# Optimization experiments

Measured on AMD Instinct MI355X. Metric: run time of the kernel, lower is better.

The kernel has to match this reference:

```python
import jax, jax.numpy as jnp
import numpy as np

EMBED_DIM = 1024
B, QL, KL = 4, 2048, 2048

def setup_inputs() -> dict:
    key = jax.random.key(0)
    k1, k2, k3, k4 = jax.random.split(key, 4)
    hidden_states = jax.random.normal(k1, (B, QL, EMBED_DIM), dtype=jnp.float32)
    decoder_hidden_states = jax.random.normal(k2, (B, KL, EMBED_DIM), dtype=jnp.float32)
    # Linear weights stored as [in, out] (torch stores [out, in]; math identical via x @ W)
    Wq = jax.random.normal(k3, (EMBED_DIM, EMBED_DIM), dtype=jnp.float32) * (1.0 / np.sqrt(EMBED_DIM))
    Wkv = jax.random.normal(k4, (EMBED_DIM, 2 * EMBED_DIM), dtype=jnp.float32) * (1.0 / np.sqrt(EMBED_DIM))
    return {"hidden_states": hidden_states, "decoder_hidden_states": decoder_hidden_states,
            "Wq": Wq, "Wkv": Wkv}

def reference(hidden_states, decoder_hidden_states, Wq, Wkv):
    d = Wq.shape[0]
    scale = 1.0 / np.sqrt(d)
    query = hidden_states @ Wq                      # [B, QL, D]
    kv = decoder_hidden_states @ Wkv                # [B, KL, 2D]
    key, value = jnp.split(kv, 2, axis=-1)          # each [B, KL, D]
    scores = jnp.einsum('bqd,bkd->bqk', query, key) * scale  # [B, QL, KL]
    w = jax.nn.softmax(scores, axis=-1)
    return jnp.einsum('bqk,bkd->bqd', w, value)     # [B, QL, D]
```

## Files before the change

kernel.cpp:

```cpp
#include <hip/hip_runtime.h>
#include <stdint.h>


typedef __bf16 bf16_t;
typedef __bf16 bf16x8 __attribute__((ext_vector_type(8)));
typedef __bf16 bf16x4 __attribute__((ext_vector_type(4)));
typedef float  f32x4  __attribute__((ext_vector_type(4)));

#define MFMA_BF16(A, B, C) __builtin_amdgcn_mfma_f32_16x16x32_bf16((A), (B), (C), 0, 0, 0)
#define ATTN_SHIFT 16.0f

__device__ __forceinline__ void async_copy16(const void* g, void* l) {
  __builtin_amdgcn_global_load_lds(
      (const __attribute__((address_space(1))) uint32_t*)g,
      (__attribute__((address_space(3))) uint32_t*)l, 16, 0, 0);
}

#define PH_PRE()                                             \
  do {                                                       \
    __builtin_amdgcn_sched_barrier(0);                       \
    __builtin_amdgcn_s_barrier();                            \
    asm volatile("s_waitcnt lgkmcnt(0)" ::: "memory");       \
    __builtin_amdgcn_sched_barrier(0);                       \
    __builtin_amdgcn_s_setprio(1);                           \
  } while (0)
#define PH_POST()                                            \
  do {                                                       \
    __builtin_amdgcn_s_setprio(0);                           \
    __builtin_amdgcn_sched_barrier(0);                       \
    __builtin_amdgcn_s_barrier();                            \
  } while (0)

__global__ void zero_f32_kernel(float* __restrict__ p, int n) {
  int i = blockIdx.x * blockDim.x + threadIdx.x;
  if (i < n) p[i] = 0.f;
}

__global__ void cast_bf16_kernel(const float* __restrict__ in, bf16_t* __restrict__ out, int n) {
  int idx = (blockIdx.x * blockDim.x + threadIdx.x) * 4;
  int stride = gridDim.x * blockDim.x * 4;
  for (int i = idx; i < n; i += stride) {
    float4 v = *(const float4*)(in + i);
    bf16x4 o;
    o[0] = (bf16_t)v.x; o[1] = (bf16_t)v.y; o[2] = (bf16_t)v.z; o[3] = (bf16_t)v.w;
    *(bf16x4*)(out + i) = o;
  }
}

__global__ void transpose_cast_kernel(const float* __restrict__ src, bf16_t* __restrict__ dst,
                                      int R, int C, float scale) {
  __shared__ float tile[32][33];
  int c0 = blockIdx.x * 32, r0 = blockIdx.y * 32;
  int tx = threadIdx.x, ty = threadIdx.y;
#pragma unroll
  for (int i = 0; i < 4; ++i) {
    int r = ty + i * 8;
    tile[r][tx] = src[(size_t)(r0 + r) * C + c0 + tx] * scale;
  }
  __syncthreads();
#pragma unroll
  for (int i = 0; i < 4; ++i) {
    int c = ty + i * 8;
    dst[(size_t)(c0 + c) * R + r0 + tx] = (bf16_t)tile[tx][c];
  }
}

template <int BN, int EPI>
__global__ __launch_bounds__(512, 2) void gemm8(
    const bf16_t* __restrict__ A, int lda, size_t sA,
    const bf16_t* __restrict__ Bt, int ldb, size_t sB,
    void* __restrict__ Cv, int ldc, size_t sC,
    void* __restrict__ Cv2, int nb, int K, float* __restrict__ rowsum) {
  constexpr int ABYTES = 256 * 64 * 2;
  constexpr int BBYTES = BN * 64 * 2;
  constexpr int NCF = BN / 64;
  __shared__ char smem[2 * ABYTES + 2 * BBYTES];

  const int bx = blockIdx.x, bz = blockIdx.z;
  const bf16_t* Ab = A + (size_t)bz * sA;
  const bf16_t* Bb = Bt + (size_t)bz * sB;
  const int m0 = (bx / nb) << 8;
  const int n0 = (bx % nb) * BN;
  const int tid = threadIdx.x, w = tid >> 6, l = tid & 63;
  const int l15 = l & 15, l4 = l >> 4;
  const int wr = w >> 2, wc = w & 3;
  const int NT = K >> 6;

  const int lrow = l >> 3;
  const int gcol = ((l & 7) ^ lrow) << 3;
  const bf16_t* PA = Ab + (size_t)(m0 + 8 * w + lrow) * lda + gcol;
  const bf16_t* PB = Bb + (size_t)(n0 + 8 * w + lrow) * ldb + gcol;

  const int sw16 = (l15 & 7) << 4;
  const int aoff0 = (wr * 128 + l15) * 128;
  const int boff0 = (wc * (BN / 4) + l15) * 128;

  f32x4 acc[8][NCF] = {};
  bf16x8 af[4][2], bfr[NCF][2];

  auto stageA = [&](int t, int h) {
    if (t >= NT) return;
    const bf16_t* s = PA + (size_t)(h * 128) * lda + (t << 6);
    char* d = smem + (t & 1) * ABYTES + h * 16384 + w * 1024;
    async_copy16(s, d);
    async_copy16(s + (size_t)64 * lda, d + 8192);
  };
  auto stageB = [&](int t, int h) {
    if (t >= NT) return;
    const bf16_t* s = PB + (size_t)(h * (BN / 2)) * ldb + (t << 6);
    char* d = smem + 2 * ABYTES + (t & 1) * BBYTES + h * (BBYTES / 2) + w * 1024;
    async_copy16(s, d);
    if constexpr (BN == 256) async_copy16(s + (size_t)64 * ldb, d + 8192);
  };

  stageB(0, 0); stageA(0, 0); stageA(0, 1); stageB(0, 1);
  __builtin_amdgcn_sched_barrier(0);
  stageB(1, 0); stageA(1, 0);
  __builtin_amdgcn_sched_barrier(0);
  if constexpr (BN == 256) asm volatile("s_waitcnt vmcnt(4)" ::: "memory");
  else                     asm volatile("s_waitcnt vmcnt(3)" ::: "memory");
  __builtin_amdgcn_s_barrier();

  for (int t = 0; t < NT; ++t) {
    const int cur = t & 1;
    const char* Ac = smem + cur * ABYTES;
    const char* Bc = smem + 2 * ABYTES + cur * BBYTES;
#pragma unroll
    for (int rf = 0; rf < 4; ++rf)
#pragma unroll
      for (int kh = 0; kh < 2; ++kh)
        af[rf][kh] = *(const bf16x8*)(Ac + aoff0 + rf * 2048 + ((((kh * 4 + l4) << 4)) ^ sw16));
#pragma unroll
    for (int cf = 0; cf < NCF / 2; ++cf)
#pragma unroll
      for (int kh = 0; kh < 2; ++kh)
        bfr[cf][kh] = *(const bf16x8*)(Bc + boff0 + cf * 2048 + ((((kh * 4 + l4) << 4)) ^ sw16));
    stageA(t + 1, 1);
    PH_PRE();
#pragma unroll
    for (int rf = 0; rf < 4; ++rf)
#pragma unroll
      for (int cf = 0; cf < NCF / 2; ++cf) {
        acc[rf][cf] = MFMA_BF16(af[rf][0], bfr[cf][0], acc[rf][cf]);
        acc[rf][cf] = MFMA_BF16(af[rf][1], bfr[cf][1], acc[rf][cf]);
      }
    PH_POST();
#pragma unroll
    for (int cf = NCF / 2; cf < NCF; ++cf)
#pragma unroll
      for (int kh = 0; kh < 2; ++kh)
        bfr[cf][kh] = *(const bf16x8*)(Bc + boff0 + cf * 2048 + ((((kh * 4 + l4) << 4)) ^ sw16));
    stageB(t + 1, 1);
    PH_PRE();
#pragma unroll
    for (int rf = 0; rf < 4; ++rf)
#pragma unroll
      for (int cf = NCF / 2; cf < NCF; ++cf) {
        acc[rf][cf] = MFMA_BF16(af[rf][0], bfr[cf][0], acc[rf][cf]);
        acc[rf][cf] = MFMA_BF16(af[rf][1], bfr[cf][1], acc[rf][cf]);
      }
    PH_POST();
#pragma unroll
    for (int rf = 0; rf < 4; ++rf)
#pragma unroll
      for (int kh = 0; kh < 2; ++kh)
        af[rf][kh] = *(const bf16x8*)(Ac + aoff0 + 8192 + rf * 2048 + ((((kh * 4 + l4) << 4)) ^ sw16));
    stageB(t + 2, 0);
    PH_PRE();
#pragma unroll
    for (int rf = 0; rf < 4; ++rf)
#pragma unroll
      for (int cf = 0; cf < NCF / 2; ++cf) {
        acc[4 + rf][cf] = MFMA_BF16(af[rf][0], bfr[cf][0], acc[4 + rf][cf]);
        acc[4 + rf][cf] = MFMA_BF16(af[rf][1], bfr[cf][1], acc[4 + rf][cf]);
      }
    PH_POST();
    stageA(t + 2, 0);
    PH_PRE();
#pragma unroll
    for (int rf = 0; rf < 4; ++rf)
#pragma unroll
      for (int cf = NCF / 2; cf < NCF; ++cf) {
        acc[4 + rf][cf] = MFMA_BF16(af[rf][0], bfr[cf][0], acc[4 + rf][cf]);
        acc[4 + rf][cf] = MFMA_BF16(af[rf][1], bfr[cf][1], acc[4 + rf][cf]);
      }
    __builtin_amdgcn_s_setprio(0);
    __builtin_amdgcn_sched_barrier(0);
    if (t < NT - 2) {
      if constexpr (BN == 256) asm volatile("s_waitcnt vmcnt(4)" ::: "memory");
      else                     asm volatile("s_waitcnt vmcnt(3)" ::: "memory");
    } else {
      asm volatile("s_waitcnt vmcnt(0)" ::: "memory");
    }
    __builtin_amdgcn_s_barrier();
  }

  __syncthreads();

  if constexpr (EPI == 0) {
    bf16_t* Cb = (bf16_t*)Cv + (size_t)bz * sC;
#pragma unroll
    for (int arf = 0; arf < 8; ++arf)
#pragma unroll
      for (int cf = 0; cf < NCF; ++cf) {
        int grow = m0 + wr * 128 + arf * 16 + l4 * 4;
        int gc = n0 + wc * (BN / 4) + cf * 16 + l15;
#pragma unroll
        for (int r = 0; r < 4; ++r)
          Cb[(size_t)(grow + r) * ldc + gc] = (bf16_t)acc[arf][cf][r];
      }
  } else if constexpr (EPI == 1) {
    bf16_t* Cb = (bf16_t*)Cv + (size_t)bz * sC;
    float* rsh = (float*)smem;
    if (tid < 256) rsh[tid] = 0.f;
    __syncthreads();
#pragma unroll
    for (int arf = 0; arf < 8; ++arf)
#pragma unroll
      for (int r = 0; r < 4; ++r) {
        int lr = wr * 128 + arf * 16 + l4 * 4 + r;
        float s = 0.f;
#pragma unroll
        for (int cf = 0; cf < NCF; ++cf) {
          float p = __expf(acc[arf][cf][r] - ATTN_SHIFT);
          bf16_t pb = (bf16_t)p;
          Cb[(size_t)(m0 + lr) * ldc + n0 + wc * (BN / 4) + cf * 16 + l15] = pb;
          s += (float)pb;
        }
        s += __shfl_xor(s, 1); s += __shfl_xor(s, 2);
        s += __shfl_xor(s, 4); s += __shfl_xor(s, 8);
        if (l15 == 0) atomicAdd(&rsh[lr], s);
      }
    __syncthreads();
    if (tid < 256) atomicAdd(&rowsum[(size_t)bz * 2048 + m0 + tid], rsh[tid]);
  } else if constexpr (EPI == 2) {
    float* rsh = (float*)smem;
    if (tid < 256) rsh[tid] = rowsum[(size_t)bz * 2048 + m0 + tid];
    __syncthreads();
    float* Cb = (float*)Cv + (size_t)bz * sC;
#pragma unroll
    for (int arf = 0; arf < 8; ++arf)
#pragma unroll
      for (int r = 0; r < 4; ++r) {
        float inv = 1.0f / rsh[wr * 128 + arf * 16 + l4 * 4 + r];
        int grow = m0 + wr * 128 + arf * 16 + l4 * 4 + r;
#pragma unroll
        for (int cf = 0; cf < NCF; ++cf)
          Cb[(size_t)grow * ldc + n0 + wc * (BN / 4) + cf * 16 + l15] = acc[arf][cf][r] * inv;
      }
  } else {
    if (n0 < 1024) {
      bf16_t* Cb = (bf16_t*)Cv;
#pragma unroll
      for (int arf = 0; arf < 8; ++arf)
#pragma unroll
        for (int cf = 0; cf < NCF; ++cf) {
          int grow = m0 + wr * 128 + arf * 16 + l4 * 4;
          int gc = n0 + wc * (BN / 4) + cf * 16 + l15;
#pragma unroll
          for (int r = 0; r < 4; ++r)
            Cb[(size_t)(grow + r) * ldc + gc] = (bf16_t)acc[arf][cf][r];
        }
    } else {
      bf16_t* VTb = (bf16_t*)Cv2;
#pragma unroll
      for (int arf = 0; arf < 8; ++arf)
#pragma unroll
        for (int cf = 0; cf < NCF; ++cf) {
          int grow0 = m0 + wr * 128 + arf * 16 + l4 * 4;
          int b = grow0 >> 11, kl = grow0 & 2047;
          int d = (n0 - 1024) + wc * (BN / 4) + cf * 16 + l15;
          bf16x4 v;
#pragma unroll
          for (int r = 0; r < 4; ++r) v[r] = (bf16_t)acc[arf][cf][r];
          *(bf16x4*)(VTb + (size_t)b * (1024 * 2048) + (size_t)d * 2048 + kl) = v;
        }
    }
  }
}

extern "C" void kernel_launch(void* const* d_in, const int* in_sizes, int n_in,
                              void* d_out, int out_size, void* d_ws, size_t ws_size,
                              hipStream_t stream) {
  const float* hs  = (const float*)d_in[0];
  const float* dhs = (const float*)d_in[1];
  const float* Wq  = (const float*)d_in[2];
  const float* Wkv = (const float*)d_in[3];
  float* out = (float*)d_out;

  const size_t M1 = 1024 * 1024;
  bf16_t* WqT  = (bf16_t*)d_ws;
  bf16_t* WkvT = WqT + M1;
  bf16_t* AB   = WkvT + 2 * M1;
  bf16_t* dhsb = AB;
  bf16_t* hsb  = AB + 8 * M1;
  bf16_t* P    = AB;
  bf16_t* Kb   = AB + 16 * M1;
  bf16_t* VTb  = Kb + 8 * M1;
  bf16_t* Qb   = VTb + 8 * M1;
  float* rowsum = (float*)(Qb + 8 * M1);

  zero_f32_kernel<<<8, 1024, 0, stream>>>(rowsum, 8192);
  cast_bf16_kernel<<<2048, 256, 0, stream>>>(dhs, dhsb, 8192 * 1024);
  cast_bf16_kernel<<<2048, 256, 0, stream>>>(hs,  hsb,  8192 * 1024);
  transpose_cast_kernel<<<dim3(32, 32), dim3(32, 8), 0, stream>>>(Wq,  WqT,  1024, 1024, 0.03125f);
  transpose_cast_kernel<<<dim3(64, 32), dim3(32, 8), 0, stream>>>(Wkv, WkvT, 1024, 2048, 1.0f);

  gemm8<256, 4><<<dim3(32 * 8, 1, 1), 512, 0, stream>>>(
      dhsb, 1024, 0, WkvT, 1024, 0, Kb, 1024, 0, VTb, 8, 1024, nullptr);
  gemm8<128, 0><<<dim3(32 * 8, 1, 1), 512, 0, stream>>>(
      hsb, 1024, 0, WqT, 1024, 0, Qb, 1024, 0, nullptr, 8, 1024, nullptr);
  gemm8<256, 1><<<dim3(64, 1, 4), 512, 0, stream>>>(
      Qb, 1024, (size_t)2048 * 1024, Kb, 1024, (size_t)2048 * 1024,
      P, 2048, (size_t)2048 * 2048, nullptr, 8, 1024, rowsum);
  gemm8<128, 2><<<dim3(64, 1, 4), 512, 0, stream>>>(
      P, 2048, (size_t)2048 * 2048, VTb, 2048, (size_t)1024 * 2048,
      out, 1024, (size_t)2048 * 1024, nullptr, 8, 2048, rowsum);
}
```

Measured before the change: 184.6 us.

## Fuse prep kernels and remap GEMM blocks across XCDs for L2 locality

Merges the rowsum zeroing and the two fp32-to-bf16 casts into one prep kernel, and the two weight transposes into one kernel, which cuts launch count. It also flattens the batch dimension into blockIdx.x and applies an XCD-aware swizzle (stride-8 interleave) so that consecutive tiles sharing A/B panels land on the same XCD's L2. The tradeoffs are extra index arithmetic and an assumption that grid size is a multiple of 8.

```diff
diff --git a/kernel.cpp b/kernel.cpp
--- a/kernel.cpp
+++ b/kernel.cpp
@@ -31,26 +31,33 @@
     __builtin_amdgcn_s_barrier();                            \
   } while (0)
 
-__global__ void zero_f32_kernel(float* __restrict__ p, int n) {
-  int i = blockIdx.x * blockDim.x + threadIdx.x;
-  if (i < n) p[i] = 0.f;
-}
-
-__global__ void cast_bf16_kernel(const float* __restrict__ in, bf16_t* __restrict__ out, int n) {
-  int idx = (blockIdx.x * blockDim.x + threadIdx.x) * 4;
+__global__ void prep_kernel(const float* __restrict__ a, const float* __restrict__ b,
+                            bf16_t* __restrict__ ab, bf16_t* __restrict__ bb,
+                            float* __restrict__ rowsum, int n) {
+  int gtid = blockIdx.x * blockDim.x + threadIdx.x;
+  if (gtid < 8192) rowsum[gtid] = 0.f;
+  int idx = gtid * 4;
   int stride = gridDim.x * blockDim.x * 4;
   for (int i = idx; i < n; i += stride) {
-    float4 v = *(const float4*)(in + i);
-    bf16x4 o;
+    float4 v = *(const float4*)(a + i);
+    float4 w = *(const float4*)(b + i);
+    bf16x4 o, p;
     o[0] = (bf16_t)v.x; o[1] = (bf16_t)v.y; o[2] = (bf16_t)v.z; o[3] = (bf16_t)v.w;
-    *(bf16x4*)(out + i) = o;
-  }
-}
-
-__global__ void transpose_cast_kernel(const float* __restrict__ src, bf16_t* __restrict__ dst,
-                                      int R, int C, float scale) {
+    p[0] = (bf16_t)w.x; p[1] = (bf16_t)w.y; p[2] = (bf16_t)w.z; p[3] = (bf16_t)w.w;
+    *(bf16x4*)(ab + i) = o;
+    *(bf16x4*)(bb + i) = p;
+  }
+}
+
+__global__ void transpose_both_kernel(const float* __restrict__ Wq, const float* __restrict__ Wkv,
+                                      bf16_t* __restrict__ WqT, bf16_t* __restrict__ WkvT) {
   __shared__ float tile[32][33];
-  int c0 = blockIdx.x * 32, r0 = blockIdx.y * 32;
+  int bx = blockIdx.x;
+  const float* src; bf16_t* dst; int R, C; float scale;
+  int cb;
+  if (bx < 32) { src = Wq;  dst = WqT;  R = 1024; C = 1024; scale = 0.03125f; cb = bx; }
+  else         { src = Wkv; dst = WkvT; R = 1024; C = 2048; scale = 1.0f;     cb = bx - 32; }
+  int c0 = cb * 32, r0 = blockIdx.y * 32;
   int tx = threadIdx.x, ty = threadIdx.y;
 #pragma unroll
   for (int i = 0; i < 4; ++i) {
@@ -70,17 +77,22 @@
     const bf16_t* __restrict__ A, int lda, size_t sA,
     const bf16_t* __restrict__ Bt, int ldb, size_t sB,
     void* __restrict__ Cv, int ldc, size_t sC,
-    void* __restrict__ Cv2, int nb, int K, float* __restrict__ rowsum) {
+    void* __restrict__ Cv2, int nb, int bpb, int K, float* __restrict__ rowsum) {
   constexpr int ABYTES = 256 * 64 * 2;
   constexpr int BBYTES = BN * 64 * 2;
   constexpr int NCF = BN / 64;
   __shared__ char smem[2 * ABYTES + 2 * BBYTES];
 
-  const int bx = blockIdx.x, bz = blockIdx.z;
+  const int bx0 = blockIdx.x;
+  const int q8 = gridDim.x >> 3;
+  const int swz = (bx0 & 7) * q8 + (bx0 >> 3);
+  const int bz = swz / bpb;
+  const int rr = swz % bpb;
+  const int m0 = (rr / nb) << 8;
+  const int n0 = (rr % nb) * BN;
+
   const bf16_t* Ab = A + (size_t)bz * sA;
   const bf16_t* Bb = Bt + (size_t)bz * sB;
-  const int m0 = (bx / nb) << 8;
-  const int n0 = (bx % nb) * BN;
   const int tid = threadIdx.x, w = tid >> 6, l = tid & 63;
   const int l15 = l & 15, l4 = l >> 4;
   const int wr = w >> 2, wc = w & 3;
@@ -300,20 +312,17 @@
   bf16_t* Qb   = VTb + 8 * M1;
   float* rowsum = (float*)(Qb + 8 * M1);
 
-  zero_f32_kernel<<<8, 1024, 0, stream>>>(rowsum, 8192);
-  cast_bf16_kernel<<<2048, 256, 0, stream>>>(dhs, dhsb, 8192 * 1024);
-  cast_bf16_kernel<<<2048, 256, 0, stream>>>(hs,  hsb,  8192 * 1024);
-  transpose_cast_kernel<<<dim3(32, 32), dim3(32, 8), 0, stream>>>(Wq,  WqT,  1024, 1024, 0.03125f);
-  transpose_cast_kernel<<<dim3(64, 32), dim3(32, 8), 0, stream>>>(Wkv, WkvT, 1024, 2048, 1.0f);
-
-  gemm8<256, 4><<<dim3(32 * 8, 1, 1), 512, 0, stream>>>(
-      dhsb, 1024, 0, WkvT, 1024, 0, Kb, 1024, 0, VTb, 8, 1024, nullptr);
-  gemm8<128, 0><<<dim3(32 * 8, 1, 1), 512, 0, stream>>>(
-      hsb, 1024, 0, WqT, 1024, 0, Qb, 1024, 0, nullptr, 8, 1024, nullptr);
-  gemm8<256, 1><<<dim3(64, 1, 4), 512, 0, stream>>>(
+  prep_kernel<<<2048, 256, 0, stream>>>(dhs, hs, dhsb, hsb, rowsum, 8192 * 1024);
+  transpose_both_kernel<<<dim3(96, 32), dim3(32, 8), 0, stream>>>(Wq, Wkv, WqT, WkvT);
+
+  gemm8<256, 4><<<256, 512, 0, stream>>>(
+      dhsb, 1024, 0, WkvT, 1024, 0, Kb, 1024, 0, VTb, 8, 256, 1024, nullptr);
+  gemm8<128, 0><<<256, 512, 0, stream>>>(
+      hsb, 1024, 0, WqT, 1024, 0, Qb, 1024, 0, nullptr, 8, 256, 1024, nullptr);
+  gemm8<256, 1><<<256, 512, 0, stream>>>(
       Qb, 1024, (size_t)2048 * 1024, Kb, 1024, (size_t)2048 * 1024,
-      P, 2048, (size_t)2048 * 2048, nullptr, 8, 1024, rowsum);
-  gemm8<128, 2><<<dim3(64, 1, 4), 512, 0, stream>>>(
+      P, 2048, (size_t)2048 * 2048, nullptr, 8, 64, 1024, rowsum);
+  gemm8<128, 2><<<256, 512, 0, stream>>>(
       P, 2048, (size_t)2048 * 2048, VTb, 2048, (size_t)1024 * 2048,
-      out, 1024, (size_t)2048 * 1024, nullptr, 8, 2048, rowsum);
-}
+      out, 1024, (size_t)2048 * 1024, nullptr, 8, 64, 2048, rowsum);
+}
```

New measurement: 167.3 us. 1.1x faster.
